# Optimization experiments

Hardware: AMD Instinct MI355X
Metric: run time of the kernel (lower is better)

The kernel has to match this reference:

```python
import jax, jax.numpy as jnp
import numpy as np

N_NODES = 50000
N_EDGES = 1600000
F_IN = 128
DIM = 128
BN_EPS = 1e-5


def setup_inputs() -> dict:
    key = jax.random.key(0)
    ks = jax.random.split(key, 8)
    x = jax.random.normal(ks[0], (N_NODES, F_IN), dtype=jnp.float32)
    edge_index = jax.random.randint(ks[1], (2, N_EDGES), 0, N_NODES, dtype=jnp.int64)
    s1 = 1.0 / np.sqrt(F_IN)
    s2 = 1.0 / np.sqrt(DIM)
    return {
        "x": x,
        "edge_index": edge_index,
        "w11": jax.random.normal(ks[2], (F_IN, DIM), dtype=jnp.float32) * s1,
        "b11": jnp.zeros((DIM,), jnp.float32),
        "w12": jax.random.normal(ks[3], (DIM, DIM), dtype=jnp.float32) * s2,
        "b12": jnp.zeros((DIM,), jnp.float32),
        "g1": jnp.ones((DIM,), jnp.float32),
        "be1": jnp.zeros((DIM,), jnp.float32),
        "w21": jax.random.normal(ks[4], (DIM, DIM), dtype=jnp.float32) * s2,
        "b21": jnp.zeros((DIM,), jnp.float32),
        "w22": jax.random.normal(ks[5], (DIM, 2), dtype=jnp.float32) * s2,
        "b22": jnp.zeros((2,), jnp.float32),
        "g2": jnp.ones((2,), jnp.float32),
        "be2": jnp.zeros((2,), jnp.float32),
    }


def _gin_conv(x, edge_index, w1, b1, w2, b2):
    # GINConv, eps=0: nn(x + sum_{(s,d) in E} x[s] scattered to d)
    src, dst = edge_index[0], edge_index[1]
    agg = jax.ops.segment_sum(x[src], dst, num_segments=N_NODES)
    h = x + agg
    h = jax.nn.relu(h @ w1 + b1)
    return h @ w2 + b2


def _batchnorm(x, gamma, beta):
    # training-mode BatchNorm1d: batch mean, biased variance, eps=1e-5
    mean = jnp.mean(x, axis=0)
    var = jnp.mean((x - mean) ** 2, axis=0)
    return (x - mean) * jax.lax.rsqrt(var + BN_EPS) * gamma + beta


def reference(x, edge_index, w11, b11, w12, b12, g1, be1,
              w21, b21, w22, b22, g2, be2):
    h = jax.nn.relu(_gin_conv(x, edge_index, w11, b11, w12, b12))
    h = _batchnorm(h, g1, be1)
    h = jax.nn.relu(_gin_conv(h, edge_index, w21, b21, w22, b22))
    h = _batchnorm(h, g2, be2)
    return h
```

## Files before the change

### kernel.cpp

```cpp
#include <hip/hip_runtime.h>

#define N_NODES 50000
#define BN_EPS 1e-5f
#define NBUCK 391
#define NCHUNK 1000
#define ENTCAP 5120

using short8 = __attribute__((ext_vector_type(8))) short;
using f32x4  = __attribute__((ext_vector_type(4))) float;

__device__ __forceinline__ float b2f(ushort h) { return __uint_as_float(((uint)h) << 16); }
__device__ __forceinline__ float blo(uint v) { return __uint_as_float(v << 16); }
__device__ __forceinline__ float bhi(uint v) { return __uint_as_float(v & 0xffff0000u); }
__device__ __forceinline__ ushort f2b(float f) {
    uint u = __float_as_uint(f);
    u += 0x7FFF + ((u >> 16) & 1);
    return (ushort)(u >> 16);
}
__device__ __forceinline__ uint packb(float lo, float hi) {
    return ((uint)f2b(hi) << 16) | (uint)f2b(lo);
}
__device__ __forceinline__ int xcd_chunk(int bid) {
    return (bid & 7) * (NCHUNK / 8) + (bid >> 3);
}

#define B_CX 6250
#define B_CW 192
#define B_Z  8
__global__ __launch_bounds__(256) void setup_kernel(const int* __restrict__ dst, int nE, int chunk,
                                                    int* __restrict__ histT,
                                                    const float4* __restrict__ x4,
                                                    ushort4* __restrict__ xb,
                                                    const float* __restrict__ w11,
                                                    const float* __restrict__ w12,
                                                    const float* __restrict__ w21,
                                                    ushort* __restrict__ o11,
                                                    ushort* __restrict__ o12,
                                                    ushort* __restrict__ o21,
                                                    float* __restrict__ statsrep) {
    __shared__ int h[NBUCK];
    const int b = blockIdx.x;
    const int tid = threadIdx.x;
    if (b < NCHUNK) {
        for (int i = tid; i < NBUCK; i += 256) h[i] = 0;
        __syncthreads();
        const int c = xcd_chunk(b);
        const int lo = c * chunk, hi = min(lo + chunk, nE);
        for (int i = lo + tid; i < hi; i += 256) atomicAdd(&h[dst[i] >> 7], 1);
        __syncthreads();
        for (int k = tid; k < NBUCK; k += 256) histT[k * NCHUNK + c] = h[k];
    } else if (b < NCHUNK + B_CX) {
        int i = (b - NCHUNK) * 256 + tid;
        float4 v = x4[i];
        ushort4 o;
        o.x = f2b(v.x); o.y = f2b(v.y); o.z = f2b(v.z); o.w = f2b(v.w);
        xb[i] = o;
    } else if (b < NCHUNK + B_CX + B_CW) {
        int id = (b - NCHUNK - B_CX) * 256 + tid;
        int m = id >> 14;
        int within = id & 16383;
        int k = within >> 7, n = within & 127;
        const float* W = (m == 0) ? w11 : (m == 1) ? w12 : w21;
        ushort* O = (m == 0) ? o11 : (m == 1) ? o12 : o21;
        O[n * 128 + k] = f2b(W[within]);
    } else {
        int i = (b - NCHUNK - B_CX - B_CW) * 256 + tid;
        if (i < 2048) statsrep[i] = 0.f;
    }
}

__global__ __launch_bounds__(256) void tot_kernel(const int* __restrict__ histT,
                                                  int* __restrict__ tot) {
    __shared__ int s[256];
    int acc = 0;
    for (int i = threadIdx.x; i < NCHUNK; i += 256) acc += histT[blockIdx.x * NCHUNK + i];
    s[threadIdx.x] = acc;
    __syncthreads();
    for (int d = 128; d > 0; d >>= 1) {
        if (threadIdx.x < d) s[threadIdx.x] += s[threadIdx.x + d];
        __syncthreads();
    }
    if (threadIdx.x == 0) tot[blockIdx.x] = s[0];
}

__global__ __launch_bounds__(1024) void base_scan_kernel(const int* __restrict__ tot,
                                                         const int* __restrict__ histT,
                                                         int* __restrict__ base_bc,
                                                         int* __restrict__ bucketbase,
                                                         int* __restrict__ rowptr, int nE) {
    __shared__ int s[1024];
    const int b = blockIdx.x;
    const int t = threadIdx.x;
    int acc = 0;
    for (int i = t; i < b; i += 1024) acc += tot[i];
    s[t] = acc;
    __syncthreads();
    for (int d = 512; d > 0; d >>= 1) {
        if (t < d) s[t] += s[t + d];
        __syncthreads();
    }
    const int bbase = s[0];
    __syncthreads();
    int v = (t < NCHUNK) ? histT[b * NCHUNK + t] : 0;
    s[t] = v;
    __syncthreads();
    for (int d = 1; d < 1024; d <<= 1) {
        int u = (t >= d) ? s[t - d] : 0;
        __syncthreads();
        s[t] += u;
        __syncthreads();
    }
    if (t < NCHUNK) base_bc[b * NCHUNK + t] = bbase + s[t] - v;
    if (t == 0) {
        bucketbase[b] = bbase;
        if (b == NBUCK - 1) bucketbase[NBUCK] = bbase + tot[b];
        if (b == 0) rowptr[N_NODES] = nE;
    }
}

__global__ __launch_bounds__(256) void place_kernel(const int* __restrict__ src,
                                                    const int* __restrict__ dst, int nE,
                                                    int chunk,
                                                    const int* __restrict__ base_bc,
                                                    uint* __restrict__ bdata) {
    __shared__ int off[NBUCK];
    const int c = xcd_chunk(blockIdx.x);
    for (int i = threadIdx.x; i < NBUCK; i += 256) off[i] = base_bc[i * NCHUNK + c];
    __syncthreads();
    const int lo = c * chunk, hi = min(lo + chunk, nE);
    for (int i = lo + threadIdx.x; i < hi; i += 256) {
        int s = src[i], d = dst[i];
        int pos = atomicAdd(&off[d >> 7], 1);
        bdata[pos] = ((uint)(d & 127) << 16) | (uint)s;
    }
}

__global__ __launch_bounds__(256) void csr_build_kernel(const int* __restrict__ bucketbase,
                                                        const uint* __restrict__ bdata,
                                                        int* __restrict__ rowptr,
                                                        ushort* __restrict__ perm, int M) {
    __shared__ uint ent[ENTCAP];
    __shared__ int hist[128];
    __shared__ int scn[128];
    __shared__ int cur[128];
    const int b = blockIdx.x;
    const int tid = threadIdx.x;
    const int bb = bucketbase[b];
    const int nb = min(bucketbase[b + 1] - bb, ENTCAP);
    if (tid < 128) hist[tid] = 0;
    for (int i = tid; i < nb; i += 256) ent[i] = bdata[bb + i];
    __syncthreads();
    for (int i = tid; i < nb; i += 256) atomicAdd(&hist[ent[i] >> 16], 1);
    __syncthreads();
    if (tid < 128) scn[tid] = hist[tid];
    __syncthreads();
    for (int d = 1; d < 128; d <<= 1) {
        int v = 0;
        if (tid < 128 && tid >= d) v = scn[tid - d];
        __syncthreads();
        if (tid < 128) scn[tid] += v;
        __syncthreads();
    }
    if (tid < 128) {
        int ex = scn[tid] - hist[tid];
        cur[tid] = ex;
        int node = b * 128 + tid;
        if (node < M) rowptr[node] = bb + ex;
    }
    __syncthreads();
    for (int i = tid; i < nb; i += 256) {
        uint e = ent[i];
        int lp = atomicAdd(&cur[e >> 16], 1);
        perm[bb + lp] = (ushort)(e & 0xffffu);
    }
}

#define ACC4(v) { acc[0] += blo(v.x); acc[1] += bhi(v.x); \
                  acc[2] += blo(v.y); acc[3] += bhi(v.y); \
                  acc[4] += blo(v.z); acc[5] += bhi(v.z); \
                  acc[6] += blo(v.w); acc[7] += bhi(v.w); }

template<bool BN>
__global__ __launch_bounds__(256) void gather_kernel(const uint4* __restrict__ xb,
                                                     const int* __restrict__ rowptr,
                                                     const ushort* __restrict__ perm,
                                                     const float* __restrict__ statsrep,
                                                     const float* __restrict__ gma,
                                                     const float* __restrict__ bta,
                                                     float invM,
                                                     uint4* __restrict__ out, int M) {
    __shared__ float scs[128], shs[128];
    if (BN) {
        if (threadIdx.x < 128) {
            int c = threadIdx.x;
            float s = 0.f, q = 0.f;
            #pragma unroll
            for (int rep = 0; rep < 8; ++rep) {
                s += statsrep[rep * 256 + c];
                q += statsrep[rep * 256 + 128 + c];
            }
            float mean = s * invM;
            float var = q * invM - mean * mean;
            float sc = rsqrtf(var + BN_EPS) * gma[c];
            scs[c] = sc;
            shs[c] = bta[c] - mean * sc;
        }
        __syncthreads();
    }
    const int node = blockIdx.x * 4 + (threadIdx.x >> 6);
    if (node >= M) return;
    const int lane = threadIdx.x & 63;
    const int g4 = lane >> 4;
    const int r = lane & 15;
    float acc[8];
    if (g4 == 0) {
        uint4 v = xb[node * 16 + r];
        acc[0] = blo(v.x); acc[1] = bhi(v.x);
        acc[2] = blo(v.y); acc[3] = bhi(v.y);
        acc[4] = blo(v.z); acc[5] = bhi(v.z);
        acc[6] = blo(v.w); acc[7] = bhi(v.w);
    } else {
        #pragma unroll
        for (int k = 0; k < 8; ++k) acc[k] = 0.f;
    }
    const int beg = rowptr[node], end = rowptr[node + 1];
    int e = beg + g4;
    while (e + 12 < end) {
        int s0 = perm[e], s1 = perm[e + 4], s2 = perm[e + 8], s3 = perm[e + 12];
        uint4 v0 = xb[s0 * 16 + r];
        uint4 v1 = xb[s1 * 16 + r];
        uint4 v2 = xb[s2 * 16 + r];
        uint4 v3 = xb[s3 * 16 + r];
        ACC4(v0); ACC4(v1); ACC4(v2); ACC4(v3);
        e += 16;
    }
    while (e + 4 < end) {
        int s0 = perm[e], s1 = perm[e + 4];
        uint4 v0 = xb[s0 * 16 + r];
        uint4 v1 = xb[s1 * 16 + r];
        ACC4(v0); ACC4(v1);
        e += 8;
    }
    if (e < end) {
        uint4 v0 = xb[(int)perm[e] * 16 + r];
        ACC4(v0);
    }
    #pragma unroll
    for (int k = 0; k < 8; ++k) {
        acc[k] += __shfl_xor(acc[k], 16);
        acc[k] += __shfl_xor(acc[k], 32);
    }
    if (g4 == 0) {
        if (BN) {
            const int f0 = r * 8;
            const float deg1 = (float)(end - beg + 1);
            #pragma unroll
            for (int k = 0; k < 8; ++k)
                acc[k] = acc[k] * scs[f0 + k] + deg1 * shs[f0 + k];
        }
        uint4 o;
        o.x = packb(acc[0], acc[1]);
        o.y = packb(acc[2], acc[3]);
        o.z = packb(acc[4], acc[5]);
        o.w = packb(acc[6], acc[7]);
        out[node * 16 + r] = o;
    }
}

__global__ __launch_bounds__(256) void mfma_mm_kernel(const ushort* __restrict__ A,
                                                      const ushort* __restrict__ Wt,
                                                      const float* __restrict__ b,
                                                      ushort* __restrict__ C, int M) {
    const int wid = threadIdx.x >> 6;
    const int lane = threadIdx.x & 63;
    const int row0 = blockIdx.x * 64 + wid * 16;
    const int r = lane & 15;
    const int kg = lane >> 4;

    const int arow = min(row0 + r, M - 1);
    const ushort* Arow = A + (size_t)arow * 128 + kg * 8;
    short8 a[4];
    #pragma unroll
    for (int kb = 0; kb < 4; ++kb)
        a[kb] = *(const short8*)(Arow + kb * 32);

    #pragma unroll
    for (int c = 0; c < 8; ++c) {
        f32x4 acc = {0.f, 0.f, 0.f, 0.f};
        const ushort* Wcol = Wt + (size_t)(c * 16 + r) * 128 + kg * 8;
        #pragma unroll
        for (int kb = 0; kb < 4; ++kb) {
            short8 bb = *(const short8*)(Wcol + kb * 32);
            acc = __builtin_amdgcn_mfma_f32_16x16x32_bf16(a[kb], bb, acc, 0, 0, 0);
        }
        float bias = b[c * 16 + r];
        #pragma unroll
        for (int j = 0; j < 4; ++j) {
            int orow = row0 + kg * 4 + j;
            if (orow < M) {
                float v = fmaxf(acc[j] + bias, 0.f);
                C[(size_t)orow * 128 + c * 16 + r] = f2b(v);
            }
        }
    }
}

__global__ __launch_bounds__(256) void mfma_mm_stats_kernel(const ushort* __restrict__ A,
                                                            const ushort* __restrict__ Wt,
                                                            const float* __restrict__ b,
                                                            ushort* __restrict__ C,
                                                            float* __restrict__ statsrep, int M) {
    const int wid = threadIdx.x >> 6;
    const int lane = threadIdx.x & 63;
    const int row0 = blockIdx.x * 64 + wid * 16;
    const int r = lane & 15;
    const int kg = lane >> 4;

    const int arow = min(row0 + r, M - 1);
    const ushort* Arow = A + (size_t)arow * 128 + kg * 8;
    short8 a[4];
    #pragma unroll
    for (int kb = 0; kb < 4; ++kb)
        a[kb] = *(const short8*)(Arow + kb * 32);

    float* sr = statsrep + (blockIdx.x & 7) * 256;
    #pragma unroll
    for (int c = 0; c < 8; ++c) {
        f32x4 acc = {0.f, 0.f, 0.f, 0.f};
        const ushort* Wcol = Wt + (size_t)(c * 16 + r) * 128 + kg * 8;
        #pragma unroll
        for (int kb = 0; kb < 4; ++kb) {
            short8 bb = *(const short8*)(Wcol + kb * 32);
            acc = __builtin_amdgcn_mfma_f32_16x16x32_bf16(a[kb], bb, acc, 0, 0, 0);
        }
        const float bias = b[c * 16 + r];
        float s = 0.f, q = 0.f;
        #pragma unroll
        for (int j = 0; j < 4; ++j) {
            int orow = row0 + kg * 4 + j;
            float v = fmaxf(acc[j] + bias, 0.f);
            if (orow < M) C[(size_t)orow * 128 + c * 16 + r] = f2b(v);
            else v = 0.f;
            s += v; q += v * v;
        }
        s += __shfl_xor(s, 16); s += __shfl_xor(s, 32);
        q += __shfl_xor(q, 16); q += __shfl_xor(q, 32);
        if (kg == 0) {
            atomicAdd(&sr[c * 16 + r], s);
            atomicAdd(&sr[128 + c * 16 + r], q);
        }
    }
}

__global__ __launch_bounds__(256) void mm2_fused_kernel(const ushort* __restrict__ A,
                                                        const ushort* __restrict__ Wt,
                                                        const float* __restrict__ b1,
                                                        const float* __restrict__ W22,
                                                        const float* __restrict__ b22,
                                                        float* __restrict__ h2,
                                                        float4* __restrict__ pblk, int M) {
    __shared__ float bred[4][4];
    const int wid = threadIdx.x >> 6;
    const int lane = threadIdx.x & 63;
    const int row0 = blockIdx.x * 64 + wid * 16;
    const int r = lane & 15;
    const int kg = lane >> 4;

    const int arow = min(row0 + r, M - 1);
    const ushort* Arow = A + (size_t)arow * 128 + kg * 8;
    short8 a[4];
    #pragma unroll
    for (int kb = 0; kb < 4; ++kb)
        a[kb] = *(const short8*)(Arow + kb * 32);

    float w2a[8], w2b[8];
    #pragma unroll
    for (int c = 0; c < 8; ++c) {
        w2a[c] = W22[(c * 16 + r) * 2 + 0];
        w2b[c] = W22[(c * 16 + r) * 2 + 1];
    }

    float s0[4] = {0.f, 0.f, 0.f, 0.f};
    float s1[4] = {0.f, 0.f, 0.f, 0.f};
    #pragma unroll
    for (int c = 0; c < 8; ++c) {
        f32x4 acc = {0.f, 0.f, 0.f, 0.f};
        const ushort* Wcol = Wt + (size_t)(c * 16 + r) * 128 + kg * 8;
        #pragma unroll
        for (int kb = 0; kb < 4; ++kb) {
            short8 bb = *(const short8*)(Wcol + kb * 32);
            acc = __builtin_amdgcn_mfma_f32_16x16x32_bf16(a[kb], bb, acc, 0, 0, 0);
        }
        float bias = b1[c * 16 + r];
        #pragma unroll
        for (int j = 0; j < 4; ++j) {
            int orow = row0 + kg * 4 + j;
            float v = fmaxf(acc[j] + bias, 0.f);
            if (orow >= M) v = 0.f;
            s0[j] += v * w2a[c];
            s1[j] += v * w2b[c];
        }
    }
    #pragma unroll
    for (int j = 0; j < 4; ++j) {
        #pragma unroll
        for (int d = 1; d < 16; d <<= 1) {
            s0[j] += __shfl_xor(s0[j], d);
            s1[j] += __shfl_xor(s1[j], d);
        }
    }
    float bs[4] = {0.f, 0.f, 0.f, 0.f};
    if (r == 0) {
        const float bb0 = b22[0], bb1 = b22[1];
        #pragma unroll
        for (int j = 0; j < 4; ++j) {
            int orow = row0 + kg * 4 + j;
            if (orow < M) {
                float o0 = fmaxf(s0[j] + bb0, 0.f);
                float o1 = fmaxf(s1[j] + bb1, 0.f);
                h2[(size_t)orow * 2 + 0] = o0;
                h2[(size_t)orow * 2 + 1] = o1;
                bs[0] += o0; bs[1] += o1; bs[2] += o0 * o0; bs[3] += o1 * o1;
            }
        }
    }
    #pragma unroll
    for (int k = 0; k < 4; ++k) {
        bs[k] += __shfl_xor(bs[k], 16);
        bs[k] += __shfl_xor(bs[k], 32);
    }
    if (lane == 0) {
        #pragma unroll
        for (int k = 0; k < 4; ++k) bred[wid][k] = bs[k];
    }
    __syncthreads();
    if (threadIdx.x == 0)
        pblk[blockIdx.x] = make_float4(bred[0][0] + bred[1][0] + bred[2][0] + bred[3][0],
                                       bred[0][1] + bred[1][1] + bred[2][1] + bred[3][1],
                                       bred[0][2] + bred[1][2] + bred[2][2] + bred[3][2],
                                       bred[0][3] + bred[1][3] + bred[2][3] + bred[3][3]);
}

__global__ __launch_bounds__(256) void bn_apply2_kernel(const float* __restrict__ h,
                                                        const float4* __restrict__ pblk, int nblk,
                                                        const float* __restrict__ gma,
                                                        const float* __restrict__ bta,
                                                        float* __restrict__ y, int n4, float invM) {
    __shared__ float4 red[256];
    const int tid = threadIdx.x;
    float4 s = make_float4(0.f, 0.f, 0.f, 0.f);
    for (int b = tid; b < nblk; b += 256) {
        float4 t = pblk[b];
        s.x += t.x; s.y += t.y; s.z += t.z; s.w += t.w;
    }
    red[tid] = s;
    __syncthreads();
    for (int d = 128; d > 0; d >>= 1) {
        if (tid < d) {
            red[tid].x += red[tid + d].x;
            red[tid].y += red[tid + d].y;
            red[tid].z += red[tid + d].z;
            red[tid].w += red[tid + d].w;
        }
        __syncthreads();
    }
    const float4 tot = red[0];
    const float m0 = tot.x * invM, m1 = tot.y * invM;
    const float v0 = tot.z * invM - m0 * m0, v1 = tot.w * invM - m1 * m1;
    const float sc0 = rsqrtf(v0 + BN_EPS) * gma[0], sc1 = rsqrtf(v1 + BN_EPS) * gma[1];
    const float sh0 = bta[0] - m0 * sc0, sh1 = bta[1] - m1 * sc1;
    int gid = blockIdx.x * 256 + tid;
    if (gid >= n4) return;
    float4 v = ((const float4*)h)[gid];
    float4 o;
    o.x = v.x * sc0 + sh0;
    o.y = v.y * sc1 + sh1;
    o.z = v.z * sc0 + sh0;
    o.w = v.w * sc1 + sh1;
    ((float4*)y)[gid] = o;
}

extern "C" void kernel_launch(void* const* d_in, const int* in_sizes, int n_in,
                              void* d_out, int out_size, void* d_ws, size_t ws_size,
                              hipStream_t stream) {
    const float* x   = (const float*)d_in[0];
    const int*   ei  = (const int*)d_in[1];
    const float* w11 = (const float*)d_in[2];
    const float* b11 = (const float*)d_in[3];
    const float* w12 = (const float*)d_in[4];
    const float* b12 = (const float*)d_in[5];
    const float* g1  = (const float*)d_in[6];
    const float* be1 = (const float*)d_in[7];
    const float* w21 = (const float*)d_in[8];
    const float* b21 = (const float*)d_in[9];
    const float* w22 = (const float*)d_in[10];
    const float* b22 = (const float*)d_in[11];
    const float* g2  = (const float*)d_in[12];
    const float* be2 = (const float*)d_in[13];

    const int M  = N_NODES;
    const int nE = in_sizes[1] / 2;
    const int* src = ei;
    const int* dst = ei + nE;
    const int chunk = (nE + NCHUNK - 1) / NCHUNK;
    const int nblk = (M + 63) / 64;

    const size_t RB = (size_t)50048 * 128 * 2;
    char* p = (char*)d_ws;
    ushort* xb   = (ushort*)p;  p += RB;
    ushort* gbuf = (ushort*)p;  p += RB;
    ushort* tbuf = (ushort*)p;  p += RB;
    ushort* hbuf = (ushort*)p;  p += RB;
    float*  h2   = (float*)p;   p += 400128;
    ushort* wt11 = (ushort*)p;  p += 32768;
    ushort* wt12 = (ushort*)p;  p += 32768;
    ushort* wt21 = (ushort*)p;  p += 32768;
    float* statsrep = (float*)p; p += 2048 * 4;
    float4* pblk = (float4*)p;  p += (size_t)nblk * 16 + 64;
    int*  histT  = (int*)p;     p += (size_t)NBUCK * NCHUNK * 4;
    int*  base_bc= (int*)p;     p += (size_t)NBUCK * NCHUNK * 4;
    int*  tot    = (int*)p;     p += 512 * 4;
    int*  bktbase= (int*)p;     p += 512 * 4;
    int*  rowptr = (int*)p;     p += (size_t)(M + 8) * 4;
    ushort* perm = (ushort*)p;  p += (size_t)nE * 2 + 64;
    uint*  bdata = (uint*)p;

    const float invM = 1.0f / (float)M;

    setup_kernel<<<NCHUNK + B_CX + B_CW + B_Z, 256, 0, stream>>>(
        dst, nE, chunk, histT, (const float4*)x, (ushort4*)xb,
        w11, w12, w21, wt11, wt12, wt21, statsrep);
    tot_kernel<<<NBUCK, 256, 0, stream>>>(histT, tot);
    base_scan_kernel<<<NBUCK, 1024, 0, stream>>>(tot, histT, base_bc, bktbase, rowptr, nE);
    place_kernel<<<NCHUNK, 256, 0, stream>>>(src, dst, nE, chunk, base_bc, bdata);
    csr_build_kernel<<<NBUCK, 256, 0, stream>>>(bktbase, bdata, rowptr, perm, M);

    gather_kernel<false><<<(M + 3) / 4, 256, 0, stream>>>((const uint4*)xb, rowptr, perm,
                                                          nullptr, nullptr, nullptr, 0.f,
                                                          (uint4*)gbuf, M);
    mfma_mm_kernel<<<nblk, 256, 0, stream>>>(gbuf, wt11, b11, tbuf, M);
    mfma_mm_stats_kernel<<<nblk, 256, 0, stream>>>(tbuf, wt12, b12, hbuf, statsrep, M);

    gather_kernel<true><<<(M + 3) / 4, 256, 0, stream>>>((const uint4*)hbuf, rowptr, perm,
                                                         statsrep, g1, be1, invM,
                                                         (uint4*)gbuf, M);
    mm2_fused_kernel<<<nblk, 256, 0, stream>>>(gbuf, wt21, b21, w22, b22, h2, pblk, M);
    bn_apply2_kernel<<<(M / 2 + 255) / 256, 256, 0, stream>>>(h2, pblk, nblk, g2, be2,
                                                              (float*)d_out, M / 2, invM);
}
```

Measured before the change: 219.2 us.

## Split gather kernel across four feature chunks with 8-lane edge groups

The neighbor-aggregation kernel now launches four times as many blocks, each handling one 32-feature slice of a node, with 8 lanes per slice reading uint2 (64-bit) loads instead of 16 lanes reading uint4. Each wavefront processes 8 edges in parallel rather than 4, which is meant to raise memory-level parallelism and shorten per-node latency chains for the random row gathers. In exchange, the perm indices and rowptr are reloaded by each of the four chunk blocks, each row read is split into smaller 64-byte segments, and the 2-edge inner unroll replaces the previous 4-edge unroll.

```diff
diff --git a/kernel.cpp b/kernel.cpp
--- a/kernel.cpp
+++ b/kernel.cpp
@@ -175,24 +175,21 @@
     }
 }
 
-#define ACC4(v) { acc[0] += blo(v.x); acc[1] += bhi(v.x); \
-                  acc[2] += blo(v.y); acc[3] += bhi(v.y); \
-                  acc[4] += blo(v.z); acc[5] += bhi(v.z); \
-                  acc[6] += blo(v.w); acc[7] += bhi(v.w); }
-
 template<bool BN>
-__global__ __launch_bounds__(256) void gather_kernel(const uint4* __restrict__ xb,
+__global__ __launch_bounds__(256) void gather_kernel(const uint2* __restrict__ xb,
                                                      const int* __restrict__ rowptr,
                                                      const ushort* __restrict__ perm,
                                                      const float* __restrict__ statsrep,
                                                      const float* __restrict__ gma,
                                                      const float* __restrict__ bta,
                                                      float invM,
-                                                     uint4* __restrict__ out, int M) {
-    __shared__ float scs[128], shs[128];
+                                                     uint2* __restrict__ out, int M) {
+    const int chunk = blockIdx.x & 3;
+    const int grp   = blockIdx.x >> 2;
+    __shared__ float scs[32], shs[32];
     if (BN) {
-        if (threadIdx.x < 128) {
-            int c = threadIdx.x;
+        if (threadIdx.x < 32) {
+            int c = chunk * 32 + threadIdx.x;
             float s = 0.f, q = 0.f;
             #pragma unroll
             for (int rep = 0; rep < 8; ++rep) {
@@ -202,68 +199,53 @@
             float mean = s * invM;
             float var = q * invM - mean * mean;
             float sc = rsqrtf(var + BN_EPS) * gma[c];
-            scs[c] = sc;
-            shs[c] = bta[c] - mean * sc;
-        }
-        __syncthreads();
-    }
-    const int node = blockIdx.x * 4 + (threadIdx.x >> 6);
+            scs[threadIdx.x] = sc;
+            shs[threadIdx.x] = bta[c] - mean * sc;
+        }
+        __syncthreads();
+    }
+    const int node = grp * 4 + (threadIdx.x >> 6);
     if (node >= M) return;
     const int lane = threadIdx.x & 63;
-    const int g4 = lane >> 4;
-    const int r = lane & 15;
-    float acc[8];
-    if (g4 == 0) {
-        uint4 v = xb[node * 16 + r];
-        acc[0] = blo(v.x); acc[1] = bhi(v.x);
-        acc[2] = blo(v.y); acc[3] = bhi(v.y);
-        acc[4] = blo(v.z); acc[5] = bhi(v.z);
-        acc[6] = blo(v.w); acc[7] = bhi(v.w);
+    const int g = lane >> 3;
+    const int r = lane & 7;
+    const int base = chunk * 8 + r;
+    float a0, a1, a2, a3;
+    if (g == 0) {
+        uint2 v = xb[node * 32 + base];
+        a0 = blo(v.x); a1 = bhi(v.x); a2 = blo(v.y); a3 = bhi(v.y);
     } else {
-        #pragma unroll
-        for (int k = 0; k < 8; ++k) acc[k] = 0.f;
+        a0 = a1 = a2 = a3 = 0.f;
     }
     const int beg = rowptr[node], end = rowptr[node + 1];
-    int e = beg + g4;
-    while (e + 12 < end) {
-        int s0 = perm[e], s1 = perm[e + 4], s2 = perm[e + 8], s3 = perm[e + 12];
-        uint4 v0 = xb[s0 * 16 + r];
-        uint4 v1 = xb[s1 * 16 + r];
-        uint4 v2 = xb[s2 * 16 + r];
-        uint4 v3 = xb[s3 * 16 + r];
-        ACC4(v0); ACC4(v1); ACC4(v2); ACC4(v3);
+    int e = beg + g;
+    while (e + 8 < end) {
+        int s0 = perm[e];
+        int s1 = perm[e + 8];
+        uint2 v0 = xb[s0 * 32 + base];
+        uint2 v1 = xb[s1 * 32 + base];
+        a0 += blo(v0.x); a1 += bhi(v0.x); a2 += blo(v0.y); a3 += bhi(v0.y);
+        a0 += blo(v1.x); a1 += bhi(v1.x); a2 += blo(v1.y); a3 += bhi(v1.y);
         e += 16;
     }
-    while (e + 4 < end) {
-        int s0 = perm[e], s1 = perm[e + 4];
-        uint4 v0 = xb[s0 * 16 + r];
-        uint4 v1 = xb[s1 * 16 + r];
-        ACC4(v0); ACC4(v1);
-        e += 8;
-    }
     if (e < end) {
-        uint4 v0 = xb[(int)perm[e] * 16 + r];
-        ACC4(v0);
-    }
-    #pragma unroll
-    for (int k = 0; k < 8; ++k) {
-        acc[k] += __shfl_xor(acc[k], 16);
-        acc[k] += __shfl_xor(acc[k], 32);
-    }
-    if (g4 == 0) {
+        uint2 v0 = xb[(int)perm[e] * 32 + base];
+        a0 += blo(v0.x); a1 += bhi(v0.x); a2 += blo(v0.y); a3 += bhi(v0.y);
+    }
+    a0 += __shfl_xor(a0, 8); a0 += __shfl_xor(a0, 16); a0 += __shfl_xor(a0, 32);
+    a1 += __shfl_xor(a1, 8); a1 += __shfl_xor(a1, 16); a1 += __shfl_xor(a1, 32);
+    a2 += __shfl_xor(a2, 8); a2 += __shfl_xor(a2, 16); a2 += __shfl_xor(a2, 32);
+    a3 += __shfl_xor(a3, 8); a3 += __shfl_xor(a3, 16); a3 += __shfl_xor(a3, 32);
+    if (g == 0) {
         if (BN) {
-            const int f0 = r * 8;
+            const int f0 = r * 4;
             const float deg1 = (float)(end - beg + 1);
-            #pragma unroll
-            for (int k = 0; k < 8; ++k)
-                acc[k] = acc[k] * scs[f0 + k] + deg1 * shs[f0 + k];
-        }
-        uint4 o;
-        o.x = packb(acc[0], acc[1]);
-        o.y = packb(acc[2], acc[3]);
-        o.z = packb(acc[4], acc[5]);
-        o.w = packb(acc[6], acc[7]);
-        out[node * 16 + r] = o;
+            a0 = a0 * scs[f0 + 0] + deg1 * shs[f0 + 0];
+            a1 = a1 * scs[f0 + 1] + deg1 * shs[f0 + 1];
+            a2 = a2 * scs[f0 + 2] + deg1 * shs[f0 + 2];
+            a3 = a3 * scs[f0 + 3] + deg1 * shs[f0 + 3];
+        }
+        out[node * 32 + base] = make_uint2(packb(a0, a1), packb(a2, a3));
     }
 }
 
@@ -504,6 +486,7 @@
     const int* dst = ei + nE;
     const int chunk = (nE + NCHUNK - 1) / NCHUNK;
     const int nblk = (M + 63) / 64;
+    const int ngrp = (M + 3) / 4;
 
     const size_t RB = (size_t)50048 * 128 * 2;
     char* p = (char*)d_ws;
@@ -535,15 +518,15 @@
     place_kernel<<<NCHUNK, 256, 0, stream>>>(src, dst, nE, chunk, base_bc, bdata);
     csr_build_kernel<<<NBUCK, 256, 0, stream>>>(bktbase, bdata, rowptr, perm, M);
 
-    gather_kernel<false><<<(M + 3) / 4, 256, 0, stream>>>((const uint4*)xb, rowptr, perm,
-                                                          nullptr, nullptr, nullptr, 0.f,
-                                                          (uint4*)gbuf, M);
+    gather_kernel<false><<<ngrp * 4, 256, 0, stream>>>((const uint2*)xb, rowptr, perm,
+                                                       nullptr, nullptr, nullptr, 0.f,
+                                                       (uint2*)gbuf, M);
     mfma_mm_kernel<<<nblk, 256, 0, stream>>>(gbuf, wt11, b11, tbuf, M);
     mfma_mm_stats_kernel<<<nblk, 256, 0, stream>>>(tbuf, wt12, b12, hbuf, statsrep, M);
 
-    gather_kernel<true><<<(M + 3) / 4, 256, 0, stream>>>((const uint4*)hbuf, rowptr, perm,
-                                                         statsrep, g1, be1, invM,
-                                                         (uint4*)gbuf, M);
+    gather_kernel<true><<<ngrp * 4, 256, 0, stream>>>((const uint2*)hbuf, rowptr, perm,
+                                                      statsrep, g1, be1, invM,
+                                                      (uint2*)gbuf, M);
     mm2_fused_kernel<<<nblk, 256, 0, stream>>>(gbuf, wt21, b21, w22, b22, h2, pblk, M);
     bn_apply2_kernel<<<(M / 2 + 255) / 256, 256, 0, stream>>>(h2, pblk, nblk, g2, be2,
                                                               (float*)d_out, M / 2, invM);
```

New measurement: 316.3 us. +44.3%, slower.
